# Kernel tuning notes

Measured on AMD Instinct MI355X. Metric: run time of the kernel, lower is better.

## Reference

```python
import jax, jax.numpy as jnp
import numpy as np
import math

MAX_L = 3
N_RBF = 8
CUTOFF = 5.5
P_CUT = 6
ZS = (1, 6, 7, 8)
N_NODES = 10000
N_EDGES = 60000
N_EMB = 3  # n_atom_basis; edge channels = N_EMB**2 = 9


def _lxlylz_list(max_l):
    lst = []
    for l in range(max_l + 1):
        for lx in range(l, -1, -1):
            for ly in range(l - lx, -1, -1):
                lst.append((lx, ly, l - lx - ly))
    return lst

LXLYLZ = _lxlylz_list(MAX_L)            # 20 monomial exponent triples
IDX = {v: i for i, v in enumerate(LXLYLZ)}
L_OF = np.array([sum(v) for v in LXLYLZ], dtype=np.int32)
LX = jnp.array([v[0] for v in LXLYLZ])
LY = jnp.array([v[1] for v in LXLYLZ])
LZ = jnp.array([v[2] for v in LXLYLZ])
L_OF_J = jnp.array(L_OF)
ZS_J = jnp.array(ZS)


def _multinom(v):
    l = sum(v)
    return math.factorial(l) // (math.factorial(v[0]) * math.factorial(v[1]) * math.factorial(v[2]))


def _splits(l):
    return [v for v in LXLYLZ if sum(v) == l]


def _nu2_terms():
    # B2_l = sum_{|lvec|=l} multinom(lvec) * A_lvec^2  (contraction of (r1.r2)^l)
    out = []
    for l in range(1, MAX_L + 1):
        vs = _splits(l)
        idx = jnp.array([IDX[v] for v in vs])
        pref = jnp.array([float(_multinom(v)) for v in vs], dtype=jnp.float32)
        out.append((idx, idx, pref))
    return out


def _nu3_terms():
    # invariants from (r1.r2)^e12 (r1.r3)^e13 (r2.r3)^e23, all e>=1, vector degrees <= MAX_L
    combos = [(a, b, c) for a in range(1, MAX_L + 1) for b in range(1, MAX_L + 1)
              for c in range(1, MAX_L + 1) if a + b <= MAX_L and a + c <= MAX_L and b + c <= MAX_L]
    out = []
    for (e12, e13, e23) in combos:
        coef = {}
        for va in _splits(e12):
            for vb in _splits(e13):
                for vc in _splits(e23):
                    v1 = (va[0] + vb[0], va[1] + vb[1], va[2] + vb[2])
                    v2 = (va[0] + vc[0], va[1] + vc[1], va[2] + vc[2])
                    v3 = (vb[0] + vc[0], vb[1] + vc[1], vb[2] + vc[2])
                    key = (v1, v2, v3)
                    coef[key] = coef.get(key, 0.0) + float(_multinom(va) * _multinom(vb) * _multinom(vc))
        keys = list(coef.keys())
        i1 = jnp.array([IDX[k[0]] for k in keys])
        i2 = jnp.array([IDX[k[1]] for k in keys])
        i3 = jnp.array([IDX[k[2]] for k in keys])
        pref = jnp.array([coef[k] for k in keys], dtype=jnp.float32)
        out.append((i1, i2, i3, pref))
    return out

NU2_TERMS = _nu2_terms()
NU3_TERMS = _nu3_terms()


def setup_inputs() -> dict:
    key = jax.random.key(0)
    k1, k2, k3, k4, k5 = jax.random.split(key, 5)
    positions = jax.random.uniform(k1, (N_NODES, 3), dtype=jnp.float32) * 4.0  # box so most r < cutoff
    atomic_numbers = ZS_J[jax.random.randint(k2, (N_NODES,), 0, len(ZS))]
    edge_index = jax.random.randint(k3, (2, N_EDGES), 0, N_NODES)
    shifts = jnp.zeros((N_EDGES, 3), jnp.float32)
    embedding_weight = jax.random.normal(k4, (len(ZS), N_EMB), jnp.float32) / np.sqrt(len(ZS))
    radial_weight = jax.random.normal(k5, (MAX_L + 1, N_RBF, N_RBF), jnp.float32) / np.sqrt(N_RBF)
    return {"positions": positions, "shifts": shifts, "embedding_weight": embedding_weight,
            "radial_weight": radial_weight, "atomic_numbers": atomic_numbers, "edge_index": edge_index}


def reference(positions, shifts, embedding_weight, radial_weight, atomic_numbers, edge_index):
    # node one-hot + embedding
    onehot = (atomic_numbers[:, None] == ZS_J[None, :]).astype(positions.dtype)
    emb = onehot @ embedding_weight                                   # [N, n_emb]
    snd, rcv = edge_index[0], edge_index[1]
    E = snd.shape[0]
    # directed edge encoding: outer product of endpoint embeddings -> [E, n_emb^2]
    enc = (emb[snd][:, :, None] * emb[rcv][:, None, :]).reshape(E, -1)
    # edge vectors / lengths (normalized)
    vec = positions[rcv] - positions[snd] + shifts
    length = jnp.maximum(jnp.linalg.norm(vec, axis=-1, keepdims=True), 1e-9)  # [E,1]
    unit = vec / length
    # Bessel RBF * polynomial cutoff
    n = jnp.arange(1, N_RBF + 1, dtype=positions.dtype)
    rbf = jnp.sqrt(2.0 / CUTOFF) * jnp.sin(n * jnp.pi * length / CUTOFF) / length  # [E,R]
    x = length / CUTOFF
    p = float(P_CUT)
    fc = (1.0 - 0.5 * (p + 1) * (p + 2) * x ** P_CUT + p * (p + 2) * x ** (P_CUT + 1)
          - 0.5 * p * (p + 1) * x ** (P_CUT + 2)) * (x < 1.0)
    radial = rbf * fc                                                  # [E,R]
    # angular monomials x^lx y^ly z^lz
    pw = unit[:, :, None] ** jnp.arange(MAX_L + 1)                     # [E,3,L+1]
    ang = pw[:, 0, LX] * pw[:, 1, LY] * pw[:, 2, LZ]                   # [E,A=20]
    # triple outer product -> per-edge attribute tensor [E,R,A,C]
    edge_attr = jnp.einsum('er,ea,ec->erac', radial, ang, enc)
    # shared per-l radial linear transform
    Wa = radial_weight[L_OF_J]                                         # [A,R,R]
    edge_attr = jnp.einsum('ars,erac->esac', Wa, edge_attr)
    # scatter-sum to receiver nodes -> A basis
    A = jax.ops.segment_sum(edge_attr, rcv, num_segments=positions.shape[0])  # [N,R,A,C]
    # symmetrizer: invariant B basis up to nu=3
    feats = [A[:, :, 0, :]]                                            # nu=1: A_{000}
    for i1, i2, pref in NU2_TERMS:
        feats.append(jnp.einsum('t,nrtc->nrc', pref, A[:, :, i1, :] * A[:, :, i2, :]))
    for i1, i2, i3, pref in NU3_TERMS:
        feats.append(jnp.einsum('t,nrtc->nrc', pref, A[:, :, i1, :] * A[:, :, i2, :] * A[:, :, i3, :]))
    return jnp.stack(feats, axis=2)                                    # [N, R, n_B=8, C]
```

## Files before the change

### kernel.cpp

```cpp
#include <hip/hip_runtime.h>

constexpr int NRBF = 8;
constexpr int NA   = 20;
constexpr int NC   = 9;
constexpr int EDW  = 64;
constexpr int CAP  = 64;
constexpr int STG  = 16;

__constant__ int cLX[NA] = {0,1,0,0,2,1,1,0,0,0,3,2,2,1,1,1,0,0,0,0};
__constant__ int cLY[NA] = {0,0,1,0,0,1,0,2,1,0,0,1,0,2,1,0,3,2,1,0};
__constant__ int cLZ[NA] = {0,0,0,1,0,0,1,0,1,2,0,0,1,0,1,2,0,1,2,3};
__constant__ int cLOF[NA]= {0,1,1,1,2,2,2,2,2,2,3,3,3,3,3,3,3,3,3,3};
constexpr int kLOF[NA]  = {0,1,1,1,2,2,2,2,2,2,3,3,3,3,3,3,3,3,3,3};

__device__ __forceinline__ int zmap(int z) {
    return z == 1 ? 0 : (z == 6 ? 1 : (z == 7 ? 2 : 3));
}

struct Nu3Tbl {
    int n;
    unsigned char i1[200], i2[200], i3[200], cb[200];
    float pref[200];
};
constexpr int idx_of(int lx, int ly, int lz) {
    int l = lx + ly + lz;
    int base = (l == 0) ? 0 : ((l == 1) ? 1 : ((l == 2) ? 4 : 10));
    int d = l - lx;
    return base + d * (d + 1) / 2 + (d - ly);
}
constexpr int factc(int k) { return k <= 1 ? 1 : k * factc(k - 1); }
constexpr float multinom(int lx, int ly, int lz) {
    return (float)(factc(lx + ly + lz) / (factc(lx) * factc(ly) * factc(lz)));
}
constexpr Nu3Tbl make_nu3() {
    Nu3Tbl t{};
    const int combos[4][3] = {{1,1,1},{1,1,2},{1,2,1},{2,1,1}};
    for (int q = 0; q < 4; ++q) {
        int e12 = combos[q][0], e13 = combos[q][1], e23 = combos[q][2];
        for (int ax = e12; ax >= 0; --ax) for (int ay = e12-ax; ay >= 0; --ay) { int az = e12-ax-ay;
        for (int bx = e13; bx >= 0; --bx) for (int by = e13-bx; by >= 0; --by) { int bz = e13-bx-by;
        for (int cx = e23; cx >= 0; --cx) for (int cy = e23-cx; cy >= 0; --cy) { int cz = e23-cx-cy;
            t.i1[t.n] = (unsigned char)idx_of(ax+bx, ay+by, az+bz);
            t.i2[t.n] = (unsigned char)idx_of(ax+cx, ay+cy, az+cz);
            t.i3[t.n] = (unsigned char)idx_of(bx+cx, by+cy, bz+cz);
            t.cb[t.n] = (unsigned char)q;
            t.pref[t.n] = multinom(ax,ay,az) * multinom(bx,by,bz) * multinom(cx,cy,cz);
            t.n++;
        }}}
    }
    return t;
}
constexpr Nu3Tbl NU3 = make_nu3();

__global__ __launch_bounds__(256) void precompute_kernel(
    const float* __restrict__ pos, const float* __restrict__ shifts,
    const float* __restrict__ embW, const float* __restrict__ radW,
    const int* __restrict__ zs, const int* __restrict__ eidx,
    float* __restrict__ edata, int* __restrict__ counts, int* __restrict__ order,
    int E)
{
    __shared__ float s_rad[4][NRBF];
    int w = threadIdx.x >> 6;
    int lane = threadIdx.x & 63;
    int e = blockIdx.x * 4 + w;
    bool valid = (e < E);

    int snd = 0, rcv = 0;
    float dx = 0.f, dy = 0.f, dz = 0.f, len = 1.f;
    if (valid) {
        snd = eidx[e]; rcv = eidx[E + e];
        dx = pos[rcv*3+0] - pos[snd*3+0] + shifts[e*3+0];
        dy = pos[rcv*3+1] - pos[snd*3+1] + shifts[e*3+1];
        dz = pos[rcv*3+2] - pos[snd*3+2] + shifts[e*3+2];
        len = fmaxf(sqrtf(dx*dx + dy*dy + dz*dz), 1e-9f);
    }
    if (valid && lane < 8) {
        float x = len * (1.0f / 5.5f);
        float fc = 0.f;
        if (x < 1.f) {
            float x2 = x * x, x6 = x2 * x2 * x2;
            fc = 1.f - 28.f * x6 + 48.f * x6 * x - 21.f * x6 * x2;
        }
        float rbf = 0.60302268915552724f *
                    sinf((float)(lane + 1) * 3.14159265358979323846f * len / 5.5f) / len;
        s_rad[w][lane] = rbf * fc;
    }
    __syncthreads();
    if (valid) {
        float v = 0.f;
        if (lane < 32) {
            int l = lane >> 3, s = lane & 7;
            float acc = 0.f;
            #pragma unroll
            for (int r = 0; r < 8; ++r) acc += radW[(l * 8 + r) * 8 + s] * s_rad[w][r];
            v = acc;
        } else if (lane < 52) {
            int a = lane - 32;
            float inv = 1.f / len;
            float ux = dx * inv, uy = dy * inv, uz = dz * inv;
            float t = 1.f;
            for (int k = 0; k < cLX[a]; ++k) t *= ux;
            for (int k = 0; k < cLY[a]; ++k) t *= uy;
            for (int k = 0; k < cLZ[a]; ++k) t *= uz;
            v = t;
        } else if (lane < 61) {
            int t = lane - 52;
            v = embW[zmap(zs[snd]) * 3 + t / 3] * embW[zmap(zs[rcv]) * 3 + t % 3];
        }
        edata[(size_t)e * EDW + lane] = v;
        if (lane == 0) {
            int p = atomicAdd(&counts[rcv], 1);
            if (p < CAP) order[rcv * CAP + p] = e;
        }
    }
}

__global__ __launch_bounds__(128) void node_kernel(
    const float* __restrict__ edata, const int* __restrict__ counts,
    const int* __restrict__ order, float* __restrict__ out, int N)
{
    int n = blockIdx.x;
    if (n >= N) return;
    __shared__ float ed[STG][EDW];
    __shared__ int   sidx[STG];
    __shared__ float Bsh[NRBF * 8 * NC];
    int tid = threadIdx.x;
    int deg = min(counts[n], CAP);

    bool active = (tid < NRBF * NC);
    int s_i = tid / NC, c_i = tid % NC;

    float Av[NA];
    #pragma unroll
    for (int a = 0; a < NA; ++a) Av[a] = 0.f;

    for (int base = 0; base < deg; base += STG) {
        int nb = min(STG, deg - base);
        if (tid < nb) sidx[tid] = order[n * CAP + base + tid];
        __syncthreads();
        for (int i = tid; i < nb * EDW; i += 128)
            ed[i >> 6][i & 63] = edata[(size_t)sidx[i >> 6] * EDW + (i & 63)];
        __syncthreads();
        if (active) {
            for (int m = 0; m < nb; ++m) {
                float ec = ed[m][52 + c_i];
                float rl[4];
                rl[0] = ed[m][ 0 + s_i] * ec;
                rl[1] = ed[m][ 8 + s_i] * ec;
                rl[2] = ed[m][16 + s_i] * ec;
                rl[3] = ed[m][24 + s_i] * ec;
                #pragma unroll
                for (int a = 0; a < NA; ++a)
                    Av[a] += rl[kLOF[a]] * ed[m][32 + a];
            }
        }
        __syncthreads();
    }

    if (active) {
        float b0 = Av[0];
        float b1 = Av[1]*Av[1] + Av[2]*Av[2] + Av[3]*Av[3];
        float b2 = Av[4]*Av[4] + 2.f*Av[5]*Av[5] + 2.f*Av[6]*Av[6]
                 + Av[7]*Av[7] + 2.f*Av[8]*Av[8] + Av[9]*Av[9];
        float b3 = Av[10]*Av[10] + 3.f*(Av[11]*Av[11] + Av[12]*Av[12] + Av[13]*Av[13])
                 + 6.f*Av[14]*Av[14] + 3.f*Av[15]*Av[15] + Av[16]*Av[16]
                 + 3.f*(Av[17]*Av[17] + Av[18]*Av[18]) + Av[19]*Av[19];
        float b4 = 0.f, b5 = 0.f, b6 = 0.f, b7 = 0.f;
        #pragma unroll
        for (int k = 0; k < NU3.n; ++k) {
            float term = NU3.pref[k] * Av[NU3.i1[k]] * Av[NU3.i2[k]] * Av[NU3.i3[k]];
            if      (NU3.cb[k] == 0) b4 += term;
            else if (NU3.cb[k] == 1) b5 += term;
            else if (NU3.cb[k] == 2) b6 += term;
            else                     b7 += term;
        }
        int sb = s_i * 8 * NC + c_i;
        Bsh[sb + 0*NC] = b0; Bsh[sb + 1*NC] = b1; Bsh[sb + 2*NC] = b2; Bsh[sb + 3*NC] = b3;
        Bsh[sb + 4*NC] = b4; Bsh[sb + 5*NC] = b5; Bsh[sb + 6*NC] = b6; Bsh[sb + 7*NC] = b7;
    }
    __syncthreads();
    float* op = out + (size_t)n * (NRBF * 8 * NC);
    for (int i = tid; i < NRBF * 8 * NC; i += 128) op[i] = Bsh[i];
}

extern "C" void kernel_launch(void* const* d_in, const int* in_sizes, int n_in,
                              void* d_out, int out_size, void* d_ws, size_t ws_size,
                              hipStream_t stream) {
    const float* pos    = (const float*)d_in[0];
    const float* shifts = (const float*)d_in[1];
    const float* embW   = (const float*)d_in[2];
    const float* radW   = (const float*)d_in[3];
    const int*   zs     = (const int*)d_in[4];
    const int*   eidx   = (const int*)d_in[5];
    float* out = (float*)d_out;

    int N = in_sizes[0] / 3;
    int E = in_sizes[5] / 2;

    float* edata = (float*)d_ws;
    int* counts  = (int*)(edata + (size_t)E * EDW);
    int* order   = counts + N;

    hipMemsetAsync(counts, 0, (size_t)N * sizeof(int), stream);

    precompute_kernel<<<dim3((E + 3) / 4), dim3(256), 0, stream>>>(
        pos, shifts, embW, radW, zs, eidx, edata, counts, order, E);

    node_kernel<<<dim3(N), dim3(128), 0, stream>>>(edata, counts, order, out, N);
}
```

Before: 129.2 us.

## Fuse per-edge feature computation into node kernel, drop edata buffer

Edge features (radial basis, angular monomials, element encoding) are no longer written to a global edata buffer. Each node block computes them for its incoming edges directly into LDS, one wavefront per edge, four edges per pass. A lightweight bucket kernel now only does the atomic receiver bucketing, and the radial values are passed between lanes with shuffles instead of shared memory plus a barrier. This removes the 64-float-per-edge global write and read, at the cost of more barriers per node and larger blocks in which only 72 of 256 threads accumulate.

```diff
diff --git a/kernel.cpp b/kernel.cpp
--- a/kernel.cpp
+++ b/kernel.cpp
@@ -5,12 +5,10 @@
 constexpr int NC   = 9;
 constexpr int EDW  = 64;
 constexpr int CAP  = 64;
-constexpr int STG  = 16;
 
 __constant__ int cLX[NA] = {0,1,0,0,2,1,1,0,0,0,3,2,2,1,1,1,0,0,0,0};
 __constant__ int cLY[NA] = {0,0,1,0,0,1,0,2,1,0,0,1,0,2,1,0,3,2,1,0};
 __constant__ int cLZ[NA] = {0,0,0,1,0,0,1,0,1,2,0,0,1,0,1,2,0,1,2,3};
-__constant__ int cLOF[NA]= {0,1,1,1,2,2,2,2,2,2,3,3,3,3,3,3,3,3,3,3};
 constexpr int kLOF[NA]  = {0,1,1,1,2,2,2,2,2,2,3,3,3,3,3,3,3,3,3,3};
 
 __device__ __forceinline__ int zmap(int z) {
@@ -52,29 +50,20 @@
 }
 constexpr Nu3Tbl NU3 = make_nu3();
 
-__global__ __launch_bounds__(256) void precompute_kernel(
-    const float* __restrict__ pos, const float* __restrict__ shifts,
+__device__ __forceinline__ void edge_to_lds(
+    int e, int lane, const float* __restrict__ pos, const float* __restrict__ shifts,
     const float* __restrict__ embW, const float* __restrict__ radW,
     const int* __restrict__ zs, const int* __restrict__ eidx,
-    float* __restrict__ edata, int* __restrict__ counts, int* __restrict__ order,
-    int E)
+    float* __restrict__ ed, int E)
 {
-    __shared__ float s_rad[4][NRBF];
-    int w = threadIdx.x >> 6;
-    int lane = threadIdx.x & 63;
-    int e = blockIdx.x * 4 + w;
-    bool valid = (e < E);
-
-    int snd = 0, rcv = 0;
-    float dx = 0.f, dy = 0.f, dz = 0.f, len = 1.f;
-    if (valid) {
-        snd = eidx[e]; rcv = eidx[E + e];
-        dx = pos[rcv*3+0] - pos[snd*3+0] + shifts[e*3+0];
-        dy = pos[rcv*3+1] - pos[snd*3+1] + shifts[e*3+1];
-        dz = pos[rcv*3+2] - pos[snd*3+2] + shifts[e*3+2];
-        len = fmaxf(sqrtf(dx*dx + dy*dy + dz*dz), 1e-9f);
-    }
-    if (valid && lane < 8) {
+    int snd = eidx[e], rcv = eidx[E + e];
+    float dx = pos[rcv*3+0] - pos[snd*3+0] + shifts[e*3+0];
+    float dy = pos[rcv*3+1] - pos[snd*3+1] + shifts[e*3+1];
+    float dz = pos[rcv*3+2] - pos[snd*3+2] + shifts[e*3+2];
+    float len = fmaxf(sqrtf(dx*dx + dy*dy + dz*dz), 1e-9f);
+
+    float myrad = 0.f;
+    if (lane < 8) {
         float x = len * (1.0f / 5.5f);
         float fc = 0.f;
         if (x < 1.f) {
@@ -83,63 +72,74 @@
         }
         float rbf = 0.60302268915552724f *
                     sinf((float)(lane + 1) * 3.14159265358979323846f * len / 5.5f) / len;
-        s_rad[w][lane] = rbf * fc;
-    }
-    __syncthreads();
-    if (valid) {
-        float v = 0.f;
-        if (lane < 32) {
-            int l = lane >> 3, s = lane & 7;
-            float acc = 0.f;
-            #pragma unroll
-            for (int r = 0; r < 8; ++r) acc += radW[(l * 8 + r) * 8 + s] * s_rad[w][r];
-            v = acc;
-        } else if (lane < 52) {
-            int a = lane - 32;
-            float inv = 1.f / len;
-            float ux = dx * inv, uy = dy * inv, uz = dz * inv;
-            float t = 1.f;
-            for (int k = 0; k < cLX[a]; ++k) t *= ux;
-            for (int k = 0; k < cLY[a]; ++k) t *= uy;
-            for (int k = 0; k < cLZ[a]; ++k) t *= uz;
-            v = t;
-        } else if (lane < 61) {
-            int t = lane - 52;
-            v = embW[zmap(zs[snd]) * 3 + t / 3] * embW[zmap(zs[rcv]) * 3 + t % 3];
-        }
-        edata[(size_t)e * EDW + lane] = v;
-        if (lane == 0) {
-            int p = atomicAdd(&counts[rcv], 1);
-            if (p < CAP) order[rcv * CAP + p] = e;
-        }
-    }
-}
-
-__global__ __launch_bounds__(128) void node_kernel(
-    const float* __restrict__ edata, const int* __restrict__ counts,
-    const int* __restrict__ order, float* __restrict__ out, int N)
+        myrad = rbf * fc;
+    }
+    float r0 = __shfl(myrad, 0), r1 = __shfl(myrad, 1), r2 = __shfl(myrad, 2),
+          r3 = __shfl(myrad, 3), r4 = __shfl(myrad, 4), r5 = __shfl(myrad, 5),
+          r6 = __shfl(myrad, 6), r7 = __shfl(myrad, 7);
+    float v = 0.f;
+    if (lane < 32) {
+        int l = lane >> 3, s = lane & 7;
+        const float* Wl = radW + l * 64 + s;
+        v = Wl[0]*r0 + Wl[8]*r1 + Wl[16]*r2 + Wl[24]*r3
+          + Wl[32]*r4 + Wl[40]*r5 + Wl[48]*r6 + Wl[56]*r7;
+    } else if (lane < 52) {
+        int a = lane - 32;
+        float inv = 1.f / len;
+        float ux = dx * inv, uy = dy * inv, uz = dz * inv;
+        float t = 1.f;
+        for (int k = 0; k < cLX[a]; ++k) t *= ux;
+        for (int k = 0; k < cLY[a]; ++k) t *= uy;
+        for (int k = 0; k < cLZ[a]; ++k) t *= uz;
+        v = t;
+    } else if (lane < 61) {
+        int t = lane - 52;
+        v = embW[zmap(zs[snd]) * 3 + t / 3] * embW[zmap(zs[rcv]) * 3 + t % 3];
+    }
+    ed[lane] = v;
+}
+
+__global__ __launch_bounds__(256) void bucket_kernel(
+    const int* __restrict__ eidx, int* __restrict__ counts,
+    int* __restrict__ order, int E)
+{
+    int e = blockIdx.x * 256 + threadIdx.x;
+    if (e >= E) return;
+    int rcv = eidx[E + e];
+    int p = atomicAdd(&counts[rcv], 1);
+    if (p < CAP) order[rcv * CAP + p] = e;
+}
+
+__global__ __launch_bounds__(256) void node_kernel(
+    const float* __restrict__ pos, const float* __restrict__ shifts,
+    const float* __restrict__ embW, const float* __restrict__ radW,
+    const int* __restrict__ zs, const int* __restrict__ eidx,
+    const int* __restrict__ counts, const int* __restrict__ order,
+    float* __restrict__ out, int N, int E)
 {
     int n = blockIdx.x;
     if (n >= N) return;
-    __shared__ float ed[STG][EDW];
-    __shared__ int   sidx[STG];
+    __shared__ float ed[4][EDW];
+    __shared__ int   sidx[CAP];
     __shared__ float Bsh[NRBF * 8 * NC];
     int tid = threadIdx.x;
     int deg = min(counts[n], CAP);
 
+    if (tid < deg) sidx[tid] = order[n * CAP + tid];
+
     bool active = (tid < NRBF * NC);
     int s_i = tid / NC, c_i = tid % NC;
+    int w = tid >> 6, lane = tid & 63;
 
     float Av[NA];
     #pragma unroll
     for (int a = 0; a < NA; ++a) Av[a] = 0.f;
-
-    for (int base = 0; base < deg; base += STG) {
-        int nb = min(STG, deg - base);
-        if (tid < nb) sidx[tid] = order[n * CAP + base + tid];
-        __syncthreads();
-        for (int i = tid; i < nb * EDW; i += 128)
-            ed[i >> 6][i & 63] = edata[(size_t)sidx[i >> 6] * EDW + (i & 63)];
+    __syncthreads();
+
+    for (int base = 0; base < deg; base += 4) {
+        int nb = min(4, deg - base);
+        if (w < nb)
+            edge_to_lds(sidx[base + w], lane, pos, shifts, embW, radW, zs, eidx, ed[w], E);
         __syncthreads();
         if (active) {
             for (int m = 0; m < nb; ++m) {
@@ -180,7 +180,7 @@
     }
     __syncthreads();
     float* op = out + (size_t)n * (NRBF * 8 * NC);
-    for (int i = tid; i < NRBF * 8 * NC; i += 128) op[i] = Bsh[i];
+    for (int i = tid; i < NRBF * 8 * NC; i += 256) op[i] = Bsh[i];
 }
 
 extern "C" void kernel_launch(void* const* d_in, const int* in_sizes, int n_in,
@@ -197,14 +197,13 @@
     int N = in_sizes[0] / 3;
     int E = in_sizes[5] / 2;
 
-    float* edata = (float*)d_ws;
-    int* counts  = (int*)(edata + (size_t)E * EDW);
-    int* order   = counts + N;
+    int* counts = (int*)d_ws;
+    int* order  = counts + N;
 
     hipMemsetAsync(counts, 0, (size_t)N * sizeof(int), stream);
 
-    precompute_kernel<<<dim3((E + 3) / 4), dim3(256), 0, stream>>>(
-        pos, shifts, embW, radW, zs, eidx, edata, counts, order, E);
-
-    node_kernel<<<dim3(N), dim3(128), 0, stream>>>(edata, counts, order, out, N);
-}
+    bucket_kernel<<<dim3((E + 255) / 256), dim3(256), 0, stream>>>(eidx, counts, order, E);
+
+    node_kernel<<<dim3(N), dim3(256), 0, stream>>>(
+        pos, shifts, embW, radW, zs, eidx, counts, order, out, N, E);
+}
```

Result: slower. 137.3 us (+6.3%).
